# Kernel tuning notes

Measured on AMD Instinct MI355X. Metric: run time of the kernel, lower is better.

The kernel has to match this reference:

```python
import jax, jax.numpy as jnp
import numpy as np

B = 65536
R = 160            # radial_len (capped at MAX_RADIAL_LEN)
EDGE_SINK_WIDTH = 8


def setup_inputs() -> dict:
    key = jax.random.key(0)
    k1, k2 = jax.random.split(key)
    return {
        "history": jax.random.uniform(k1, (B, R, 3), dtype=jnp.float32),
        "color_rgb": jax.random.uniform(k2, (B, 3), dtype=jnp.float32),
        "offset_per_frame_60hz": jnp.float32(1.3),
        "persistence_per_frame_60hz": jnp.float32(0.92),
        "diffusion01": jnp.float32(0.5),
        "dt_seconds": jnp.float32(1.0 / 60.0),
        "amount01": jnp.float32(0.8),
        "spread01": jnp.float32(0.4),
    }


def _forward(history, color_rgb, offset, persistence, diffusion01, dt_seconds, amount01, spread01):
    dt = jnp.clip(dt_seconds, 0.0, 0.05)
    dt_scale = dt * 60.0
    dt_offset = offset * dt_scale
    dt_persist = persistence ** dt_scale

    # ---- inject at centre: 5-bin spread kernel, then clamp to [0,1] ----
    amount = jnp.clip(amount01, 0.0, 1.0)
    spread = jnp.clip(spread01, 0.0, 1.0)
    energy = color_rgb * amount                      # [B,3]
    tight = 1.0 - spread
    w = jnp.stack([0.5 + 0.4 * tight,
                   0.2 * spread + 0.05,
                   0.12 * spread,
                   0.06 * spread,
                   0.02 * spread])                   # [5]
    h = history.at[:, :5, :].add(energy[:, None, :] * w[None, :, None])
    h = jnp.clip(h, 0.0, 1.0)

    # ---- semi-Lagrangian push advection (vectorized scatter-add) ----
    i = jnp.arange(R, dtype=h.dtype)                 # source bin positions
    new_pos = i + dt_offset
    valid = (new_pos >= 0.0) & (new_pos < R - 1)     # bins outside are dropped
    left = jnp.clip(jnp.floor(new_pos).astype(jnp.int32), 0, R - 2)
    frac = new_pos - left.astype(h.dtype)
    wl = jnp.where(valid, (1.0 - frac) * dt_persist, 0.0)  # [R]
    wr = jnp.where(valid, frac * dt_persist, 0.0)
    work = jnp.zeros_like(h)
    work = work.at[:, left, :].add(h * wl[None, :, None])
    work = work.at[:, left + 1, :].add(h * wr[None, :, None])
    h = work

    # ---- diffusion: [k, 1-2k, k] stencil with ZERO boundary taps ----
    k = 0.15 * diffusion01
    c = 1.0 - 2.0 * k
    padded = jnp.pad(h, ((0, 0), (1, 1), (0, 0)))    # zero pad matches torch boundary
    h = c * h + k * padded[:, :-2, :] + k * padded[:, 2:, :]

    # ---- quadratic edge sink over last EDGE_SINK_WIDTH bins ----
    idx = jnp.arange(R)
    t = (R - 1 - idx).astype(h.dtype) / float(EDGE_SINK_WIDTH)
    fade = jnp.where(idx >= R - EDGE_SINK_WIDTH, t * t, jnp.ones((), h.dtype))
    h = h * fade[None, :, None]
    return h


def reference(history, color_rgb, offset_per_frame_60hz, persistence_per_frame_60hz,
              diffusion01, dt_seconds, amount01, spread01):
    return _forward(history, color_rgb, offset_per_frame_60hz,
                    persistence_per_frame_60hz, diffusion01, dt_seconds,
                    amount01, spread01)
```

## Files before the change

kernel.cpp:

```cpp
#include <hip/hip_runtime.h>
#include <math.h>

#define RBINS 160
#define BROWS 65536
#define ROWELEMS 480
#define ROWF4 (ROWELEMS / 4)
#define TASKS_PER_ROW 20
#define NTHREADS 256
#define NBLOCKS_MAIN ((BROWS * TASKS_PER_ROW) / NTHREADS)
#define NBLOCKS_FIX (BROWS / NTHREADS)

__device__ __forceinline__ float clamp01(float x) {
    return __builtin_amdgcn_fmed3f(x, 0.0f, 1.0f);
}

__device__ __forceinline__ void store4(float* p, float a, float b, float c, float d) {
    *(float4*)p = make_float4(a, b, c, d);
}

template<int P, int H>
__device__ __forceinline__ void stencil_half(
    const float* __restrict__ w,
    float u1, float u2, float u3, float u4,
    float* __restrict__ r)
{
    #pragma unroll
    for (int m = 0; m < 12; ++m) {
        const int base = P + 12 * H + m;
        float acc = u1 * w[base];
        acc = fmaf(u2, w[base + 3], acc);
        acc = fmaf(u3, w[base + 6], acc);
        acc = fmaf(u4, w[base + 9], acc);
        r[m] = acc;
    }
}

template<int P>
__device__ __forceinline__ void compute_store24(
    const float* __restrict__ w,
    float u1, float u2, float u3, float u4,
    float* __restrict__ outp, bool fadeq, int bin0)
{
    float r[12];
    stencil_half<P, 0>(w, u1, u2, u3, u4, r);
    if (fadeq) {
        #pragma unroll
        for (int mb = 0; mb < 4; ++mb) {
            const int j = bin0 + mb;
            const float t = (float)(RBINS - 1 - j) * 0.125f;
            const float ff = (j >= RBINS - 8) ? t * t : 1.0f;
            r[3*mb+0] *= ff; r[3*mb+1] *= ff; r[3*mb+2] *= ff;
        }
    }
    store4(outp + 0, r[0], r[1], r[2],  r[3]);
    store4(outp + 4, r[4], r[5], r[6],  r[7]);
    store4(outp + 8, r[8], r[9], r[10], r[11]);

    stencil_half<P, 1>(w, u1, u2, u3, u4, r);
    if (fadeq) {
        #pragma unroll
        for (int mb = 0; mb < 4; ++mb) {
            const int j = bin0 + 4 + mb;
            const float t = (float)(RBINS - 1 - j) * 0.125f;
            const float ff = (j >= RBINS - 8) ? t * t : 1.0f;
            r[3*mb+0] *= ff; r[3*mb+1] *= ff; r[3*mb+2] *= ff;
        }
    }
    store4(outp + 12, r[0], r[1], r[2],  r[3]);
    store4(outp + 16, r[4], r[5], r[6],  r[7]);
    store4(outp + 20, r[8], r[9], r[10], r[11]);
}

__device__ __forceinline__ void inject36(
    float* __restrict__ w, int a0,
    const float* __restrict__ color, int b,
    float aw0, float aw1, float aw2, float aw3, float aw4)
{
    const float c0 = color[3*b+0];
    const float c1 = color[3*b+1];
    const float c2 = color[3*b+2];
    #pragma unroll
    for (int u = 0; u < 36; ++u) {
        const int f = a0 + u;
        if ((unsigned)f < 15u) {
            const int bin = f / 3;
            const int ch  = f - 3 * bin;
            const float cv = (ch == 0) ? c0 : (ch == 1) ? c1 : c2;
            const float av = (bin == 0) ? aw0 : (bin == 1) ? aw1 :
                             (bin == 2) ? aw2 : (bin == 3) ? aw3 : aw4;
            w[u] += cv * av;
        }
    }
}

__global__ __launch_bounds__(NTHREADS, 4) void beat_kernel(
    const float* __restrict__ hist,
    const float* __restrict__ color,
    const float* __restrict__ p_offset,
    const float* __restrict__ p_persist,
    const float* __restrict__ p_diff,
    const float* __restrict__ p_dt,
    const float* __restrict__ p_amount,
    const float* __restrict__ p_spread,
    float* __restrict__ out)
{
    const float offs = *p_offset;
    const float pers = *p_persist;
    const float diff = *p_diff;
    const float dts  = *p_dt;

    const float dt       = fminf(fmaxf(dts, 0.0f), 0.05f);
    const float dt_scale = dt * 60.0f;
    const float s        = offs * dt_scale;
    const float dt_pers  = __powf(pers, dt_scale);
    const int   dfl      = (int)floorf(s);
    const float frac     = s - (float)dfl;
    const float kk = 0.15f * diff;
    const float cc = 1.0f - 2.0f * kk;
    const float wl = (1.0f - frac) * dt_pers;
    const float wr = frac * dt_pers;
    const float u1 = wr * kk;
    const float u2 = fmaf(wl, kk, wr * cc);
    const float u3 = fmaf(wl, cc, wr * kk);
    const float u4 = wl * kk;

    const int ilo = max(0, (int)ceilf(-s));
    const int ihi = min(RBINS - 1, (int)ceilf((float)(RBINS - 1) - s) - 1);
    const int flo = 3 * ilo;
    const int fhi = 3 * ihi + 3;

    int b, c, A;
    bool is_fix;
    if (blockIdx.x < NBLOCKS_MAIN) {
        const int task = blockIdx.x * NTHREADS + threadIdx.x;
        b = task / TASKS_PER_ROW;
        c = task - b * TASKS_PER_ROW;
        A = c * 24 - 6 - 3 * dfl;
        if (A < 15 && c < 1) return;
        is_fix = false;
    } else {
        b = (blockIdx.x - NBLOCKS_MAIN) * NTHREADS + threadIdx.x;
        c = 0;
        A = -6 - 3 * dfl;
        is_fix = true;
    }

    const int e0 = c * 24;
    const int p  = A & 3;
    const int a0 = A - p;
    const int q0 = a0 >> 2;

    const float4* src4 = (const float4*)hist + (size_t)b * ROWF4;
    #define CLQ(q) min(max(q0 + (q), 0), ROWF4 - 1)
    const float4 v0 = src4[CLQ(0)];
    const float4 v1 = src4[CLQ(1)];
    const float4 v2 = src4[CLQ(2)];
    const float4 v3 = src4[CLQ(3)];
    const float4 v4 = src4[CLQ(4)];
    const float4 v5 = src4[CLQ(5)];
    const float4 v6 = src4[CLQ(6)];
    const float4 v7 = src4[CLQ(7)];
    const float4 v8 = src4[CLQ(8)];
    #undef CLQ

    float w[36];
    w[0]=v0.x; w[1]=v0.y; w[2]=v0.z; w[3]=v0.w;
    w[4]=v1.x; w[5]=v1.y; w[6]=v1.z; w[7]=v1.w;
    w[8]=v2.x; w[9]=v2.y; w[10]=v2.z; w[11]=v2.w;
    w[12]=v3.x; w[13]=v3.y; w[14]=v3.z; w[15]=v3.w;
    w[16]=v4.x; w[17]=v4.y; w[18]=v4.z; w[19]=v4.w;
    w[20]=v5.x; w[21]=v5.y; w[22]=v5.z; w[23]=v5.w;
    w[24]=v6.x; w[25]=v6.y; w[26]=v6.z; w[27]=v6.w;
    w[28]=v7.x; w[29]=v7.y; w[30]=v7.z; w[31]=v7.w;
    w[32]=v8.x; w[33]=v8.y; w[34]=v8.z; w[35]=v8.w;

    if (A < 15) {
        const float am = fminf(fmaxf(*p_amount, 0.0f), 1.0f);
        const float sp = fminf(fmaxf(*p_spread, 0.0f), 1.0f);
        const float tight = 1.0f - sp;
        inject36(w, a0, color, b,
                 am * fmaf(0.4f, tight, 0.5f), am * fmaf(0.2f, sp, 0.05f),
                 am * (0.12f * sp), am * (0.06f * sp), am * (0.02f * sp));
    }

    const int lo_u = flo - a0;
    const int hi_u = fhi - a0;
    #pragma unroll
    for (int u = 0; u < 36; ++u) {
        const bool v = (u >= lo_u) && (u < hi_u);
        w[u] = v ? clamp01(w[u]) : 0.0f;
    }

    if (is_fix && A >= 15) return;

    float* outp = out + (size_t)b * ROWELEMS + e0;
    const bool fadeq = (c == TASKS_PER_ROW - 1);
    const int bin0 = 8 * c;
    switch (p) {
        case 0:  compute_store24<0>(w, u1, u2, u3, u4, outp, fadeq, bin0); break;
        case 1:  compute_store24<1>(w, u1, u2, u3, u4, outp, fadeq, bin0); break;
        case 2:  compute_store24<2>(w, u1, u2, u3, u4, outp, fadeq, bin0); break;
        default: compute_store24<3>(w, u1, u2, u3, u4, outp, fadeq, bin0); break;
    }
}

extern "C" void kernel_launch(void* const* d_in, const int* in_sizes, int n_in,
                              void* d_out, int out_size, void* d_ws, size_t ws_size,
                              hipStream_t stream) {
    const float* hist      = (const float*)d_in[0];
    const float* color     = (const float*)d_in[1];
    const float* p_offset  = (const float*)d_in[2];
    const float* p_persist = (const float*)d_in[3];
    const float* p_diff    = (const float*)d_in[4];
    const float* p_dt      = (const float*)d_in[5];
    const float* p_amount  = (const float*)d_in[6];
    const float* p_spread  = (const float*)d_in[7];
    float* outp = (float*)d_out;

    beat_kernel<<<dim3(NBLOCKS_MAIN + NBLOCKS_FIX), dim3(NTHREADS), 0, stream>>>(
        hist, color, p_offset, p_persist, p_diff, p_dt, p_amount, p_spread, outp);
}
```

Baseline: 250.3 us.

## Stage row tiles through LDS with coalesced loads and apply injection during staging

Each block now cooperatively loads 16 full rows into shared memory with coalesced float4 reads, adding the centre injection while staging. Each thread then reads its overlapping 9-float4 window from LDS instead of global memory, with a skewed index to reduce bank conflicts. This removes the separate fix-up blocks and the redundant overlapping global reads, at the cost of a barrier and LDS capacity per block, which may limit occupancy.

```diff
diff --git a/kernel.cpp b/kernel.cpp
--- a/kernel.cpp
+++ b/kernel.cpp
@@ -4,19 +4,19 @@
 #define RBINS 160
 #define BROWS 65536
 #define ROWELEMS 480
-#define ROWF4 (ROWELEMS / 4)
-#define TASKS_PER_ROW 20
-#define NTHREADS 256
-#define NBLOCKS_MAIN ((BROWS * TASKS_PER_ROW) / NTHREADS)
-#define NBLOCKS_FIX (BROWS / NTHREADS)
+#define ROWF4 120
+#define TILE_ROWS 16
+#define TILE_F4 (TILE_ROWS * ROWF4)
+#define NTHREADS 320
+#define NBLOCKS (BROWS / TILE_ROWS)
+#define SROUNDS (TILE_F4 / NTHREADS)
+#define LDS_SLOTS 2159
 
 __device__ __forceinline__ float clamp01(float x) {
     return __builtin_amdgcn_fmed3f(x, 0.0f, 1.0f);
 }
 
-__device__ __forceinline__ void store4(float* p, float a, float b, float c, float d) {
-    *(float4*)p = make_float4(a, b, c, d);
-}
+__device__ __forceinline__ int swz(int q) { return q + (q >> 3); }
 
 template<int P, int H>
 __device__ __forceinline__ void stencil_half(
@@ -52,9 +52,9 @@
             r[3*mb+0] *= ff; r[3*mb+1] *= ff; r[3*mb+2] *= ff;
         }
     }
-    store4(outp + 0, r[0], r[1], r[2],  r[3]);
-    store4(outp + 4, r[4], r[5], r[6],  r[7]);
-    store4(outp + 8, r[8], r[9], r[10], r[11]);
+    *(float4*)(outp + 0) = make_float4(r[0], r[1], r[2],  r[3]);
+    *(float4*)(outp + 4) = make_float4(r[4], r[5], r[6],  r[7]);
+    *(float4*)(outp + 8) = make_float4(r[8], r[9], r[10], r[11]);
 
     stencil_half<P, 1>(w, u1, u2, u3, u4, r);
     if (fadeq) {
@@ -66,29 +66,26 @@
             r[3*mb+0] *= ff; r[3*mb+1] *= ff; r[3*mb+2] *= ff;
         }
     }
-    store4(outp + 12, r[0], r[1], r[2],  r[3]);
-    store4(outp + 16, r[4], r[5], r[6],  r[7]);
-    store4(outp + 20, r[8], r[9], r[10], r[11]);
-}
-
-__device__ __forceinline__ void inject36(
-    float* __restrict__ w, int a0,
-    const float* __restrict__ color, int b,
+    *(float4*)(outp + 12) = make_float4(r[0], r[1], r[2],  r[3]);
+    *(float4*)(outp + 16) = make_float4(r[4], r[5], r[6],  r[7]);
+    *(float4*)(outp + 20) = make_float4(r[8], r[9], r[10], r[11]);
+}
+
+__device__ __forceinline__ void inject4(
+    float4& v, int c4, float cl0, float cl1, float cl2,
     float aw0, float aw1, float aw2, float aw3, float aw4)
 {
-    const float c0 = color[3*b+0];
-    const float c1 = color[3*b+1];
-    const float c2 = color[3*b+2];
+    float* vp = (float*)&v;
     #pragma unroll
-    for (int u = 0; u < 36; ++u) {
-        const int f = a0 + u;
-        if ((unsigned)f < 15u) {
+    for (int k = 0; k < 4; ++k) {
+        const int f = 4 * c4 + k;
+        if (f < 15) {
             const int bin = f / 3;
             const int ch  = f - 3 * bin;
-            const float cv = (ch == 0) ? c0 : (ch == 1) ? c1 : c2;
+            const float cv = (ch == 0) ? cl0 : (ch == 1) ? cl1 : cl2;
             const float av = (bin == 0) ? aw0 : (bin == 1) ? aw1 :
                              (bin == 2) ? aw2 : (bin == 3) ? aw3 : aw4;
-            w[u] += cv * av;
+            vp[k] += cv * av;
         }
     }
 }
@@ -104,6 +101,11 @@
     const float* __restrict__ p_spread,
     float* __restrict__ out)
 {
+    __shared__ float4 tile[LDS_SLOTS];
+
+    const int tid  = threadIdx.x;
+    const int row0 = blockIdx.x * TILE_ROWS;
+
     const float offs = *p_offset;
     const float pers = *p_persist;
     const float diff = *p_diff;
@@ -129,72 +131,79 @@
     const int flo = 3 * ilo;
     const int fhi = 3 * ihi + 3;
 
-    int b, c, A;
-    bool is_fix;
-    if (blockIdx.x < NBLOCKS_MAIN) {
-        const int task = blockIdx.x * NTHREADS + threadIdx.x;
-        b = task / TASKS_PER_ROW;
-        c = task - b * TASKS_PER_ROW;
-        A = c * 24 - 6 - 3 * dfl;
-        if (A < 15 && c < 1) return;
-        is_fix = false;
-    } else {
-        b = (blockIdx.x - NBLOCKS_MAIN) * NTHREADS + threadIdx.x;
-        c = 0;
-        A = -6 - 3 * dfl;
-        is_fix = true;
-    }
-
+    const float am = fminf(fmaxf(*p_amount, 0.0f), 1.0f);
+    const float sp = fminf(fmaxf(*p_spread, 0.0f), 1.0f);
+    const float tight = 1.0f - sp;
+    const float aw0 = am * fmaf(0.4f, tight, 0.5f);
+    const float aw1 = am * fmaf(0.2f, sp, 0.05f);
+    const float aw2 = am * (0.12f * sp);
+    const float aw3 = am * (0.06f * sp);
+    const float aw4 = am * (0.02f * sp);
+
+    {
+        const float4* src4 = (const float4*)hist + (size_t)row0 * ROWF4;
+        const int i0 = tid;
+        const int i1 = tid + 1 * NTHREADS;
+        const int i2 = tid + 2 * NTHREADS;
+        const int i3 = tid + 3 * NTHREADS;
+        const int i4 = tid + 4 * NTHREADS;
+        const int i5 = tid + 5 * NTHREADS;
+        float4 v0 = src4[i0];
+        float4 v1 = src4[i1];
+        float4 v2 = src4[i2];
+        float4 v3 = src4[i3];
+        float4 v4 = src4[i4];
+        float4 v5 = src4[i5];
+
+        #define STAGE(K)                                                     \
+        {                                                                    \
+            const int i  = i##K;                                             \
+            const int rr = i / ROWF4;                                        \
+            const int c4 = i - rr * ROWF4;                                   \
+            if (c4 < 4) {                                                    \
+                const float* cp = color + 3 * (row0 + rr);                   \
+                inject4(v##K, c4, cp[0], cp[1], cp[2],                       \
+                        aw0, aw1, aw2, aw3, aw4);                            \
+            }                                                                \
+            tile[swz(i)] = v##K;                                             \
+        }
+        STAGE(0) STAGE(1) STAGE(2) STAGE(3) STAGE(4) STAGE(5)
+        #undef STAGE
+    }
+    __syncthreads();
+
+    const int r  = tid / 20;
+    const int c  = tid - r * 20;
     const int e0 = c * 24;
+    const int A  = e0 - 6 - 3 * dfl;
     const int p  = A & 3;
     const int a0 = A - p;
-    const int q0 = a0 >> 2;
-
-    const float4* src4 = (const float4*)hist + (size_t)b * ROWF4;
-    #define CLQ(q) min(max(q0 + (q), 0), ROWF4 - 1)
-    const float4 v0 = src4[CLQ(0)];
-    const float4 v1 = src4[CLQ(1)];
-    const float4 v2 = src4[CLQ(2)];
-    const float4 v3 = src4[CLQ(3)];
-    const float4 v4 = src4[CLQ(4)];
-    const float4 v5 = src4[CLQ(5)];
-    const float4 v6 = src4[CLQ(6)];
-    const float4 v7 = src4[CLQ(7)];
-    const float4 v8 = src4[CLQ(8)];
-    #undef CLQ
+    const int qc = a0 >> 2;
+    const int base = r * ROWF4;
 
     float w[36];
-    w[0]=v0.x; w[1]=v0.y; w[2]=v0.z; w[3]=v0.w;
-    w[4]=v1.x; w[5]=v1.y; w[6]=v1.z; w[7]=v1.w;
-    w[8]=v2.x; w[9]=v2.y; w[10]=v2.z; w[11]=v2.w;
-    w[12]=v3.x; w[13]=v3.y; w[14]=v3.z; w[15]=v3.w;
-    w[16]=v4.x; w[17]=v4.y; w[18]=v4.z; w[19]=v4.w;
-    w[20]=v5.x; w[21]=v5.y; w[22]=v5.z; w[23]=v5.w;
-    w[24]=v6.x; w[25]=v6.y; w[26]=v6.z; w[27]=v6.w;
-    w[28]=v7.x; w[29]=v7.y; w[30]=v7.z; w[31]=v7.w;
-    w[32]=v8.x; w[33]=v8.y; w[34]=v8.z; w[35]=v8.w;
-
-    if (A < 15) {
-        const float am = fminf(fmaxf(*p_amount, 0.0f), 1.0f);
-        const float sp = fminf(fmaxf(*p_spread, 0.0f), 1.0f);
-        const float tight = 1.0f - sp;
-        inject36(w, a0, color, b,
-                 am * fmaf(0.4f, tight, 0.5f), am * fmaf(0.2f, sp, 0.05f),
-                 am * (0.12f * sp), am * (0.06f * sp), am * (0.02f * sp));
+    #pragma unroll
+    for (int j = 0; j < 9; ++j) {
+        const int qj = min(max(qc + j, 0), ROWF4 - 1);
+        const float4 v = tile[swz(base + qj)];
+        w[4*j+0] = v.x; w[4*j+1] = v.y; w[4*j+2] = v.z; w[4*j+3] = v.w;
     }
 
     const int lo_u = flo - a0;
     const int hi_u = fhi - a0;
-    #pragma unroll
-    for (int u = 0; u < 36; ++u) {
-        const bool v = (u >= lo_u) && (u < hi_u);
-        w[u] = v ? clamp01(w[u]) : 0.0f;
-    }
-
-    if (is_fix && A >= 15) return;
-
-    float* outp = out + (size_t)b * ROWELEMS + e0;
-    const bool fadeq = (c == TASKS_PER_ROW - 1);
+    if (lo_u > 0 || hi_u < 36) {
+        #pragma unroll
+        for (int u = 0; u < 36; ++u) {
+            const bool v = (u >= lo_u) && (u < hi_u);
+            w[u] = v ? clamp01(w[u]) : 0.0f;
+        }
+    } else {
+        #pragma unroll
+        for (int u = 0; u < 36; ++u) w[u] = clamp01(w[u]);
+    }
+
+    float* outp = out + (size_t)(row0 + r) * ROWELEMS + e0;
+    const bool fadeq = (c == 19);
     const int bin0 = 8 * c;
     switch (p) {
         case 0:  compute_store24<0>(w, u1, u2, u3, u4, outp, fadeq, bin0); break;
@@ -217,6 +226,6 @@
     const float* p_spread  = (const float*)d_in[7];
     float* outp = (float*)d_out;
 
-    beat_kernel<<<dim3(NBLOCKS_MAIN + NBLOCKS_FIX), dim3(NTHREADS), 0, stream>>>(
+    beat_kernel<<<dim3(NBLOCKS), dim3(NTHREADS), 0, stream>>>(
         hist, color, p_offset, p_persist, p_diff, p_dt, p_amount, p_spread, outp);
 }
```

Result: faster. 244.4 us (-2.4%).

## Process two rows per thread with batched loads and interleaved compute

Applied to the files above, without the earlier changes.

Each main-path thread now handles the same 24-element chunk for two adjacent rows. It issues all 18 float4 loads up front, and a sched_barrier keeps them ahead of the compute. The compute and stores are then interleaved in halves across the two rows. This halves the main grid and is meant to raise memory-level parallelism per thread and amortise the scalar setup. The cost is higher register pressure, which may reduce occupancy, and load addresses that are less coalesced across the two rows.

```diff
diff --git a/kernel.cpp b/kernel.cpp
--- a/kernel.cpp
+++ b/kernel.cpp
@@ -4,18 +4,14 @@
 #define RBINS 160
 #define BROWS 65536
 #define ROWELEMS 480
-#define ROWF4 (ROWELEMS / 4)
+#define ROWF4 120
 #define TASKS_PER_ROW 20
 #define NTHREADS 256
-#define NBLOCKS_MAIN ((BROWS * TASKS_PER_ROW) / NTHREADS)
+#define NBLOCKS_MAIN ((BROWS / 2 * TASKS_PER_ROW) / NTHREADS)
 #define NBLOCKS_FIX (BROWS / NTHREADS)
 
 __device__ __forceinline__ float clamp01(float x) {
     return __builtin_amdgcn_fmed3f(x, 0.0f, 1.0f);
-}
-
-__device__ __forceinline__ void store4(float* p, float a, float b, float c, float d) {
-    *(float4*)p = make_float4(a, b, c, d);
 }
 
 template<int P, int H>
@@ -35,43 +31,41 @@
     }
 }
 
-template<int P>
-__device__ __forceinline__ void compute_store24(
+template<int P, int H>
+__device__ __forceinline__ void st12(
     const float* __restrict__ w,
     float u1, float u2, float u3, float u4,
     float* __restrict__ outp, bool fadeq, int bin0)
 {
     float r[12];
-    stencil_half<P, 0>(w, u1, u2, u3, u4, r);
+    stencil_half<P, H>(w, u1, u2, u3, u4, r);
     if (fadeq) {
         #pragma unroll
         for (int mb = 0; mb < 4; ++mb) {
-            const int j = bin0 + mb;
+            const int j = bin0 + 4 * H + mb;
             const float t = (float)(RBINS - 1 - j) * 0.125f;
             const float ff = (j >= RBINS - 8) ? t * t : 1.0f;
             r[3*mb+0] *= ff; r[3*mb+1] *= ff; r[3*mb+2] *= ff;
         }
     }
-    store4(outp + 0, r[0], r[1], r[2],  r[3]);
-    store4(outp + 4, r[4], r[5], r[6],  r[7]);
-    store4(outp + 8, r[8], r[9], r[10], r[11]);
-
-    stencil_half<P, 1>(w, u1, u2, u3, u4, r);
-    if (fadeq) {
-        #pragma unroll
-        for (int mb = 0; mb < 4; ++mb) {
-            const int j = bin0 + 4 + mb;
-            const float t = (float)(RBINS - 1 - j) * 0.125f;
-            const float ff = (j >= RBINS - 8) ? t * t : 1.0f;
-            r[3*mb+0] *= ff; r[3*mb+1] *= ff; r[3*mb+2] *= ff;
-        }
-    }
-    store4(outp + 12, r[0], r[1], r[2],  r[3]);
-    store4(outp + 16, r[4], r[5], r[6],  r[7]);
-    store4(outp + 20, r[8], r[9], r[10], r[11]);
-}
-
-__device__ __forceinline__ void inject36(
+    *(float4*)(outp + 12*H + 0) = make_float4(r[0], r[1], r[2],  r[3]);
+    *(float4*)(outp + 12*H + 4) = make_float4(r[4], r[5], r[6],  r[7]);
+    *(float4*)(outp + 12*H + 8) = make_float4(r[8], r[9], r[10], r[11]);
+}
+
+template<int LO, int HI>
+__device__ __forceinline__ void maskclamp(
+    float* __restrict__ w, int lo_u, int hi_u)
+{
+    #pragma unroll
+    for (int u = LO; u < HI; ++u) {
+        const bool v = (u >= lo_u) && (u < hi_u);
+        w[u] = v ? clamp01(w[u]) : 0.0f;
+    }
+}
+
+template<int LO, int HI>
+__device__ __forceinline__ void injseg(
     float* __restrict__ w, int a0,
     const float* __restrict__ color, int b,
     float aw0, float aw1, float aw2, float aw3, float aw4)
@@ -80,7 +74,7 @@
     const float c1 = color[3*b+1];
     const float c2 = color[3*b+2];
     #pragma unroll
-    for (int u = 0; u < 36; ++u) {
+    for (int u = LO; u < HI; ++u) {
         const int f = a0 + u;
         if ((unsigned)f < 15u) {
             const int bin = f / 3;
@@ -91,6 +85,75 @@
             w[u] += cv * av;
         }
     }
+}
+
+__device__ __forceinline__ void fill24(
+    float* __restrict__ w,
+    float4 v0, float4 v1, float4 v2, float4 v3, float4 v4, float4 v5)
+{
+    w[0]=v0.x;  w[1]=v0.y;  w[2]=v0.z;  w[3]=v0.w;
+    w[4]=v1.x;  w[5]=v1.y;  w[6]=v1.z;  w[7]=v1.w;
+    w[8]=v2.x;  w[9]=v2.y;  w[10]=v2.z; w[11]=v2.w;
+    w[12]=v3.x; w[13]=v3.y; w[14]=v3.z; w[15]=v3.w;
+    w[16]=v4.x; w[17]=v4.y; w[18]=v4.z; w[19]=v4.w;
+    w[20]=v5.x; w[21]=v5.y; w[22]=v5.z; w[23]=v5.w;
+}
+
+__device__ __forceinline__ void fillhi(
+    float* __restrict__ w, float4 v6, float4 v7, float4 v8)
+{
+    w[24]=v6.x; w[25]=v6.y; w[26]=v6.z; w[27]=v6.w;
+    w[28]=v7.x; w[29]=v7.y; w[30]=v7.z; w[31]=v7.w;
+    w[32]=v8.x; w[33]=v8.y; w[34]=v8.z; w[35]=v8.w;
+}
+
+template<int P>
+__device__ __forceinline__ void pipeline2(
+    float4 A0, float4 A1, float4 A2, float4 A3, float4 A4, float4 A5,
+    float4 A6, float4 A7, float4 A8,
+    float4 B0, float4 B1, float4 B2, float4 B3, float4 B4, float4 B5,
+    float4 B6, float4 B7, float4 B8,
+    int a0, int Ae, int lo_u, int hi_u,
+    float u1, float u2, float u3, float u4,
+    bool fadeq, int bin0,
+    float* __restrict__ outA, float* __restrict__ outB,
+    const float* __restrict__ color, int b0,
+    const float* __restrict__ p_amount, const float* __restrict__ p_spread)
+{
+    float aw0 = 0, aw1 = 0, aw2 = 0, aw3 = 0, aw4 = 0;
+    const bool inj = (Ae < 15);
+    if (inj) {
+        const float am = fminf(fmaxf(*p_amount, 0.0f), 1.0f);
+        const float sp = fminf(fmaxf(*p_spread, 0.0f), 1.0f);
+        const float tight = 1.0f - sp;
+        aw0 = am * fmaf(0.4f, tight, 0.5f);
+        aw1 = am * fmaf(0.2f, sp, 0.05f);
+        aw2 = am * (0.12f * sp);
+        aw3 = am * (0.06f * sp);
+        aw4 = am * (0.02f * sp);
+    }
+
+    float wA[36], wB[36];
+
+    fill24(wA, A0, A1, A2, A3, A4, A5);
+    if (inj) injseg<0, 24>(wA, a0, color, b0, aw0, aw1, aw2, aw3, aw4);
+    maskclamp<0, 24>(wA, lo_u, hi_u);
+    st12<P, 0>(wA, u1, u2, u3, u4, outA, fadeq, bin0);
+
+    fill24(wB, B0, B1, B2, B3, B4, B5);
+    if (inj) injseg<0, 24>(wB, a0, color, b0 + 1, aw0, aw1, aw2, aw3, aw4);
+    maskclamp<0, 24>(wB, lo_u, hi_u);
+    st12<P, 0>(wB, u1, u2, u3, u4, outB, fadeq, bin0);
+
+    fillhi(wA, A6, A7, A8);
+    if (inj) injseg<24, 36>(wA, a0, color, b0, aw0, aw1, aw2, aw3, aw4);
+    maskclamp<24, 36>(wA, lo_u, hi_u);
+    st12<P, 1>(wA, u1, u2, u3, u4, outA, fadeq, bin0);
+
+    fillhi(wB, B6, B7, B8);
+    if (inj) injseg<24, 36>(wB, a0, color, b0 + 1, aw0, aw1, aw2, aw3, aw4);
+    maskclamp<24, 36>(wB, lo_u, hi_u);
+    st12<P, 1>(wB, u1, u2, u3, u4, outB, fadeq, bin0);
 }
 
 __global__ __launch_bounds__(NTHREADS, 4) void beat_kernel(
@@ -129,78 +192,103 @@
     const int flo = 3 * ilo;
     const int fhi = 3 * ihi + 3;
 
-    int b, c, A;
-    bool is_fix;
     if (blockIdx.x < NBLOCKS_MAIN) {
         const int task = blockIdx.x * NTHREADS + threadIdx.x;
-        b = task / TASKS_PER_ROW;
-        c = task - b * TASKS_PER_ROW;
-        A = c * 24 - 6 - 3 * dfl;
-        if (A < 15 && c < 1) return;
-        is_fix = false;
+        const int pr = task / TASKS_PER_ROW;
+        const int c  = task - pr * TASKS_PER_ROW;
+        const int b0 = 2 * pr;
+        const int e0 = c * 24;
+        const int A  = e0 - 6 - 3 * dfl;
+        if (A < 15 && c == 0) return;
+        const int p  = A & 3;
+        const int a0 = A - p;
+        const int q0 = a0 >> 2;
+
+        #define CLQ(q) min(max(q0 + (q), 0), ROWF4 - 1)
+        const int i0 = CLQ(0), i1 = CLQ(1), i2 = CLQ(2), i3 = CLQ(3),
+                  i4 = CLQ(4), i5 = CLQ(5), i6 = CLQ(6), i7 = CLQ(7), i8 = CLQ(8);
+        #undef CLQ
+
+        const float4* s0_ = (const float4*)hist + (size_t)b0 * ROWF4;
+        const float4* s1_ = s0_ + ROWF4;
+        const float4 A0 = s0_[i0], A1 = s0_[i1], A2 = s0_[i2], A3 = s0_[i3],
+                     A4 = s0_[i4], A5 = s0_[i5], A6 = s0_[i6], A7 = s0_[i7],
+                     A8 = s0_[i8];
+        const float4 B0 = s1_[i0], B1 = s1_[i1], B2 = s1_[i2], B3 = s1_[i3],
+                     B4 = s1_[i4], B5 = s1_[i5], B6 = s1_[i6], B7 = s1_[i7],
+                     B8 = s1_[i8];
+        __builtin_amdgcn_sched_barrier(0);
+
+        const int lo_u = flo - a0;
+        const int hi_u = fhi - a0;
+        float* outA = out + (size_t)b0 * ROWELEMS + e0;
+        float* outB = outA + ROWELEMS;
+        const bool fadeq = (c == TASKS_PER_ROW - 1);
+        const int bin0 = 8 * c;
+
+        switch (p) {
+            case 0:  pipeline2<0>(A0,A1,A2,A3,A4,A5,A6,A7,A8,
+                                  B0,B1,B2,B3,B4,B5,B6,B7,B8,
+                                  a0, A, lo_u, hi_u, u1,u2,u3,u4,
+                                  fadeq, bin0, outA, outB, color, b0,
+                                  p_amount, p_spread); break;
+            case 1:  pipeline2<1>(A0,A1,A2,A3,A4,A5,A6,A7,A8,
+                                  B0,B1,B2,B3,B4,B5,B6,B7,B8,
+                                  a0, A, lo_u, hi_u, u1,u2,u3,u4,
+                                  fadeq, bin0, outA, outB, color, b0,
+                                  p_amount, p_spread); break;
+            case 2:  pipeline2<2>(A0,A1,A2,A3,A4,A5,A6,A7,A8,
+                                  B0,B1,B2,B3,B4,B5,B6,B7,B8,
+                                  a0, A, lo_u, hi_u, u1,u2,u3,u4,
+                                  fadeq, bin0, outA, outB, color, b0,
+                                  p_amount, p_spread); break;
+            default: pipeline2<3>(A0,A1,A2,A3,A4,A5,A6,A7,A8,
+                                  B0,B1,B2,B3,B4,B5,B6,B7,B8,
+                                  a0, A, lo_u, hi_u, u1,u2,u3,u4,
+                                  fadeq, bin0, outA, outB, color, b0,
+                                  p_amount, p_spread); break;
+        }
     } else {
-        b = (blockIdx.x - NBLOCKS_MAIN) * NTHREADS + threadIdx.x;
-        c = 0;
-        A = -6 - 3 * dfl;
-        is_fix = true;
-    }
-
-    const int e0 = c * 24;
-    const int p  = A & 3;
-    const int a0 = A - p;
-    const int q0 = a0 >> 2;
-
-    const float4* src4 = (const float4*)hist + (size_t)b * ROWF4;
-    #define CLQ(q) min(max(q0 + (q), 0), ROWF4 - 1)
-    const float4 v0 = src4[CLQ(0)];
-    const float4 v1 = src4[CLQ(1)];
-    const float4 v2 = src4[CLQ(2)];
-    const float4 v3 = src4[CLQ(3)];
-    const float4 v4 = src4[CLQ(4)];
-    const float4 v5 = src4[CLQ(5)];
-    const float4 v6 = src4[CLQ(6)];
-    const float4 v7 = src4[CLQ(7)];
-    const float4 v8 = src4[CLQ(8)];
-    #undef CLQ
-
-    float w[36];
-    w[0]=v0.x; w[1]=v0.y; w[2]=v0.z; w[3]=v0.w;
-    w[4]=v1.x; w[5]=v1.y; w[6]=v1.z; w[7]=v1.w;
-    w[8]=v2.x; w[9]=v2.y; w[10]=v2.z; w[11]=v2.w;
-    w[12]=v3.x; w[13]=v3.y; w[14]=v3.z; w[15]=v3.w;
-    w[16]=v4.x; w[17]=v4.y; w[18]=v4.z; w[19]=v4.w;
-    w[20]=v5.x; w[21]=v5.y; w[22]=v5.z; w[23]=v5.w;
-    w[24]=v6.x; w[25]=v6.y; w[26]=v6.z; w[27]=v6.w;
-    w[28]=v7.x; w[29]=v7.y; w[30]=v7.z; w[31]=v7.w;
-    w[32]=v8.x; w[33]=v8.y; w[34]=v8.z; w[35]=v8.w;
-
-    if (A < 15) {
+        const int b = (blockIdx.x - NBLOCKS_MAIN) * NTHREADS + threadIdx.x;
+        const int A = -6 - 3 * dfl;
+        if (A >= 15) return;
+        const int p  = A & 3;
+        const int a0 = A - p;
+        const int q0 = a0 >> 2;
+
+        const float4* src4 = (const float4*)hist + (size_t)b * ROWF4;
+        #define CLQ(q) min(max(q0 + (q), 0), ROWF4 - 1)
+        const float4 v0 = src4[CLQ(0)], v1 = src4[CLQ(1)], v2 = src4[CLQ(2)],
+                     v3 = src4[CLQ(3)], v4 = src4[CLQ(4)], v5 = src4[CLQ(5)],
+                     v6 = src4[CLQ(6)], v7 = src4[CLQ(7)], v8 = src4[CLQ(8)];
+        #undef CLQ
+
+        float w[36];
+        fill24(w, v0, v1, v2, v3, v4, v5);
+        fillhi(w, v6, v7, v8);
+
         const float am = fminf(fmaxf(*p_amount, 0.0f), 1.0f);
         const float sp = fminf(fmaxf(*p_spread, 0.0f), 1.0f);
         const float tight = 1.0f - sp;
-        inject36(w, a0, color, b,
-                 am * fmaf(0.4f, tight, 0.5f), am * fmaf(0.2f, sp, 0.05f),
-                 am * (0.12f * sp), am * (0.06f * sp), am * (0.02f * sp));
-    }
-
-    const int lo_u = flo - a0;
-    const int hi_u = fhi - a0;
-    #pragma unroll
-    for (int u = 0; u < 36; ++u) {
-        const bool v = (u >= lo_u) && (u < hi_u);
-        w[u] = v ? clamp01(w[u]) : 0.0f;
-    }
-
-    if (is_fix && A >= 15) return;
-
-    float* outp = out + (size_t)b * ROWELEMS + e0;
-    const bool fadeq = (c == TASKS_PER_ROW - 1);
-    const int bin0 = 8 * c;
-    switch (p) {
-        case 0:  compute_store24<0>(w, u1, u2, u3, u4, outp, fadeq, bin0); break;
-        case 1:  compute_store24<1>(w, u1, u2, u3, u4, outp, fadeq, bin0); break;
-        case 2:  compute_store24<2>(w, u1, u2, u3, u4, outp, fadeq, bin0); break;
-        default: compute_store24<3>(w, u1, u2, u3, u4, outp, fadeq, bin0); break;
+        injseg<0, 36>(w, a0, color, b,
+                      am * fmaf(0.4f, tight, 0.5f), am * fmaf(0.2f, sp, 0.05f),
+                      am * (0.12f * sp), am * (0.06f * sp), am * (0.02f * sp));
+
+        const int lo_u = flo - a0;
+        const int hi_u = fhi - a0;
+        maskclamp<0, 36>(w, lo_u, hi_u);
+
+        float* outp = out + (size_t)b * ROWELEMS;
+        switch (p) {
+            case 0:  st12<0,0>(w, u1,u2,u3,u4, outp, false, 0);
+                     st12<0,1>(w, u1,u2,u3,u4, outp, false, 0); break;
+            case 1:  st12<1,0>(w, u1,u2,u3,u4, outp, false, 0);
+                     st12<1,1>(w, u1,u2,u3,u4, outp, false, 0); break;
+            case 2:  st12<2,0>(w, u1,u2,u3,u4, outp, false, 0);
+                     st12<2,1>(w, u1,u2,u3,u4, outp, false, 0); break;
+            default: st12<3,0>(w, u1,u2,u3,u4, outp, false, 0);
+                     st12<3,1>(w, u1,u2,u3,u4, outp, false, 0); break;
+        }
     }
 }
 
```

Result: slower. 276.4 us (+10.4%).
